# Kernel tuning notes

Hardware: AMD Instinct MI355X
Metric: run time of the kernel (lower is better)

## Reference

```python
import jax, jax.numpy as jnp
import numpy as np

N, E, G = 40000, 400000, 64
IN, ED, HID, HEADS, OUT = 2, 18, 64, 4, 3

def _glorot(key, shape):
    fan_in = shape[0]
    return jax.random.normal(key, shape, dtype=jnp.float32) / np.float32(np.sqrt(fan_in))

def setup_inputs():
    key = jax.random.key(0)
    ks = jax.random.split(key, 32)
    d1 = HEADS * HID  # 256
    return {
        "x": jax.random.normal(ks[0], (N, IN), jnp.float32),
        "edge_index": jax.random.randint(ks[1], (2, E), 0, N),
        "edge_attr": jax.random.normal(ks[2], (E, ED), jnp.float32),
        "batch": jnp.sort(jax.random.randint(ks[3], (N,), 0, G)),
        # conv1: TransformerConv(2 -> 64, heads=4, concat=True, beta=True, edge_dim=18)
        "Wq1": _glorot(ks[4], (IN, d1)), "bq1": jnp.zeros((d1,), jnp.float32),
        "Wk1": _glorot(ks[5], (IN, d1)), "bk1": jnp.zeros((d1,), jnp.float32),
        "Wv1": _glorot(ks[6], (IN, d1)), "bv1": jnp.zeros((d1,), jnp.float32),
        "We1": _glorot(ks[7], (ED, d1)),
        "Wskip1": _glorot(ks[8], (IN, d1)), "bskip1": jnp.zeros((d1,), jnp.float32),
        "Wbeta1": _glorot(ks[9], (3 * d1, 1)),
        # conv2: TransformerConv(256 -> 64, heads=1, concat=False, beta=True, edge_dim=18)
        "Wq2": _glorot(ks[10], (d1, HID)), "bq2": jnp.zeros((HID,), jnp.float32),
        "Wk2": _glorot(ks[11], (d1, HID)), "bk2": jnp.zeros((HID,), jnp.float32),
        "Wv2": _glorot(ks[12], (d1, HID)), "bv2": jnp.zeros((HID,), jnp.float32),
        "We2": _glorot(ks[13], (ED, HID)),
        "Wskip2": _glorot(ks[14], (d1, HID)), "bskip2": jnp.zeros((HID,), jnp.float32),
        "Wbeta2": _glorot(ks[15], (3 * HID, 1)),
        "Wlin": _glorot(ks[16], (HID, OUT)), "blin": jnp.zeros((OUT,), jnp.float32),
    }

def _tconv(x, src, dst, edge_attr, Wq, bq, Wk, bk, Wv, bv, We, Wskip, bskip, Wbeta, H, C, concat):
    # PyG TransformerConv with edge_dim, beta=True, root_weight=True (eval: dropout off)
    n = x.shape[0]
    q = (x @ Wq + bq).reshape(n, H, C)
    k = (x @ Wk + bk).reshape(n, H, C)
    v = (x @ Wv + bv).reshape(n, H, C)
    e = (edge_attr @ We).reshape(-1, H, C)              # [E,H,C]
    kj = k[src] + e                                      # key_j + edge
    alpha = jnp.einsum('ehc,ehc->eh', q[dst], kj) * (1.0 / (C ** 0.5))  # [E,H]
    # segment softmax over destination nodes
    amax = jax.ops.segment_max(alpha, dst, num_segments=n)
    ex = jnp.exp(alpha - amax[dst])
    den = jax.ops.segment_sum(ex, dst, num_segments=n)
    w = ex / (den[dst] + 1e-16)
    msg = (v[src] + e) * w[:, :, None]                   # [E,H,C]
    out = jax.ops.segment_sum(msg, dst, num_segments=n)  # [N,H,C]
    out = out.reshape(n, H * C) if concat else out.mean(axis=1)
    # beta-gated skip connection
    xr = x @ Wskip + bskip
    beta = jax.nn.sigmoid(jnp.concatenate([out, xr, out - xr], axis=-1) @ Wbeta)
    return beta * xr + (1.0 - beta) * out

def reference(x, edge_index, edge_attr, batch, Wq1, bq1, Wk1, bk1, Wv1, bv1, We1, Wskip1, bskip1, Wbeta1, Wq2, bq2, Wk2, bk2, Wv2, bv2, We2, Wskip2, bskip2, Wbeta2, Wlin, blin):
    src, dst = edge_index[0], edge_index[1]
    h = jax.nn.relu(_tconv(x, src, dst, edge_attr, Wq1, bq1, Wk1, bk1, Wv1, bv1, We1, Wskip1, bskip1, Wbeta1, HEADS, HID, True))
    h = jax.nn.relu(_tconv(h, src, dst, edge_attr, Wq2, bq2, Wk2, bk2, Wv2, bv2, We2, Wskip2, bskip2, Wbeta2, 1, HID, False))
    # global mean pool per graph
    s = jax.ops.segment_sum(h, batch, num_segments=G)
    cnt = jax.ops.segment_sum(jnp.ones((h.shape[0], 1), h.dtype), batch, num_segments=G)
    pooled = s / jnp.maximum(cnt, 1.0)
    return pooled @ Wlin + blin
```

## Files before the change

kernel.cpp:

```cpp
#include <hip/hip_runtime.h>
#include <hip/hip_fp16.h>

#define N_NODES 40000
#define N_EDGES 400000
#define N_GRAPHS 64
#define D1 256
#define HIDC 64
#define NHEADS 4
#define EDIM 18
#define EPAD 20
#define OUTF 3
#define APAD 264

typedef _Float16 f16x8 __attribute__((ext_vector_type(8)));
typedef float f32x4 __attribute__((ext_vector_type(4)));

__global__ void prep_w(const float* __restrict__ Wq, const float* __restrict__ bq,
                       const float* __restrict__ Wk, const float* __restrict__ bk,
                       const float* __restrict__ Wv, const float* __restrict__ bv,
                       const float* __restrict__ Ws, const float* __restrict__ bs,
                       const float* __restrict__ We2,
                       const float* __restrict__ Wq1, const float* __restrict__ bq1,
                       const float* __restrict__ Wk1, const float* __restrict__ bk1,
                       const float* __restrict__ We1,
                       __half* __restrict__ Bt, float* __restrict__ bias,
                       float* __restrict__ cbuf) {
    int c = blockIdx.x, k = threadIdx.x;
    if (c < 256) {
        int m = c >> 6, d = c & 63;
        const float* W = (m == 0) ? Wq : (m == 1) ? Wk : (m == 2) ? Wv : Ws;
        Bt[c * 256 + k] = __float2half(W[k * 64 + d]);
        if (k == 0) {
            const float* b = (m == 0) ? bq : (m == 1) ? bk : (m == 2) ? bv : bs;
            bias[c] = b[d];
        }
    } else if (c < 288) {
        int j = c - 256;
        float s = 0.f;
        if (j < EDIM)
            for (int cc = 0; cc < 64; ++cc) s += Wq[k * 64 + cc] * We2[j * 64 + cc];
        Bt[c * 256 + k] = __float2half(s);
        if (k == 0) {
            float b = 0.f;
            if (j < EDIM)
                for (int cc = 0; cc < 64; ++cc) b += bq[cc] * We2[j * 64 + cc];
            bias[c] = b;
        }
    } else {
        int t = k;
        if (t < 36) {
            int h = t / 9, r = t % 9, a = r / 3, b = r % 3;
            const float* A = (a == 0) ? Wq1 : (a == 1) ? Wq1 + D1 : bq1;
            const float* B = (b == 0) ? Wk1 : (b == 1) ? Wk1 + D1 : bk1;
            float s = 0.f;
            for (int cc = 0; cc < 64; ++cc) s += A[h * 64 + cc] * B[h * 64 + cc];
            cbuf[h * 63 + a * 3 + b] = s;
        } else if (t < 252) {
            int i = t - 36;
            int h = i / 54, rr = (i % 54) / 18, j = i % 18;
            const float* A = (rr == 0) ? Wq1 : (rr == 1) ? Wq1 + D1 : bq1;
            float s = 0.f;
            for (int cc = 0; cc < 64; ++cc) s += A[h * 64 + cc] * We1[j * D1 + h * 64 + cc];
            cbuf[h * 63 + 9 + rr * 18 + j] = s;
        }
    }
}

__global__ void initA(const float* __restrict__ x, const float* __restrict__ cbuf,
                      float* __restrict__ coef, float* __restrict__ acc1,
                      float* __restrict__ acc2, float* __restrict__ out2,
                      int* __restrict__ deg, float* __restrict__ pooled,
                      int* __restrict__ gs, int* __restrict__ ge) {
    int t = blockIdx.x * 256 + threadIdx.x;
    acc1[t] = 0.f;
    {
        int n = t / 84, r = t % 84, h = r / 21, c = r % 21;
        const float* cb = cbuf + h * 63;
        float x0 = x[2 * n], x1 = x[2 * n + 1], o;
        if (c < 3) o = x0 * cb[c] + x1 * cb[3 + c] + cb[6 + c];
        else { int j = c - 3; o = x0 * cb[9 + j] + x1 * cb[27 + j] + cb[45 + j]; }
        coef[t] = o;
    }
    if (t < N_NODES * 64) out2[t] = 0.f;
    if (t < N_NODES * 20) acc2[t] = 0.f;
    if (t < N_NODES) deg[t] = 0;
    if (t < N_GRAPHS * HIDC) pooled[t] = 0.f;
    if (t < N_GRAPHS) { gs[t] = 0; ge[t] = 0; }
}

__global__ void hist_kernel(const int* __restrict__ ei, int* __restrict__ deg,
                            const int* __restrict__ batch, int* __restrict__ gs,
                            int* __restrict__ ge) {
    int e = blockIdx.x * 256 + threadIdx.x;
    if (e < N_EDGES) atomicAdd(&deg[ei[N_EDGES + e]], 1);
    int n = e;
    if (n < N_NODES) {
        int b = batch[n];
        if (n == 0) gs[b] = 0;
        else { int pb = batch[n - 1]; if (pb != b) { ge[pb] = n; gs[b] = n; } }
        if (n == N_NODES - 1) ge[b] = N_NODES;
    }
}

__global__ void scanA(const int* __restrict__ deg, int* __restrict__ bsum) {
    __shared__ int s[256];
    int b = blockIdx.x, t = threadIdx.x;
    s[t] = (t < 160) ? deg[b * 160 + t] : 0;
    __syncthreads();
    for (int off = 128; off; off >>= 1) {
        if (t < off) s[t] += s[t + off];
        __syncthreads();
    }
    if (t == 0) bsum[b] = s[0];
}

__global__ void scanB(const int* __restrict__ bsum, int* __restrict__ boff) {
    __shared__ int s[256];
    int t = threadIdx.x;
    int v = (t < 250) ? bsum[t] : 0;
    s[t] = v;
    __syncthreads();
    for (int off = 1; off < 256; off <<= 1) {
        int add = (t >= off) ? s[t - off] : 0;
        __syncthreads();
        s[t] += add;
        __syncthreads();
    }
    if (t < 250) boff[t] = s[t] - v;
}

__global__ void scanC(const int* __restrict__ deg, const int* __restrict__ boff,
                      int* __restrict__ cursor) {
    __shared__ int s[256];
    int b = blockIdx.x, t = threadIdx.x;
    int v = (t < 160) ? deg[b * 160 + t] : 0;
    s[t] = v;
    __syncthreads();
    for (int off = 1; off < 256; off <<= 1) {
        int add = (t >= off) ? s[t - off] : 0;
        __syncthreads();
        s[t] += add;
        __syncthreads();
    }
    if (t < 160) cursor[b * 160 + t] = boff[b] + s[t] - v;
}

__global__ void perm_kernel(const int* __restrict__ ei, int* __restrict__ cursor,
                            int* __restrict__ inv) {
    int e = blockIdx.x * 256 + threadIdx.x;
    if (e >= N_EDGES) return;
    int p = atomicAdd(&cursor[ei[N_EDGES + e]], 1);
    inv[p] = e;
}

__global__ void gatherE(const int* __restrict__ inv, const int* __restrict__ ei,
                        const float* __restrict__ ea, const float* __restrict__ x,
                        const float* __restrict__ coef,
                        int* __restrict__ src_s, int* __restrict__ dst_s,
                        float* __restrict__ ea_s, float* __restrict__ alpha1) {
    int p = blockIdx.x * 256 + threadIdx.x;
    if (p >= N_EDGES) return;
    int e = inv[p];
    int src = ei[e], dst = ei[N_EDGES + e];
    src_s[p] = src;
    dst_s[p] = dst;
    const float* srow = ea + (size_t)e * EDIM;
    float s[EDIM];
    #pragma unroll
    for (int j = 0; j < EDIM; ++j) s[j] = srow[j];
    float x0 = x[src * 2], x1 = x[src * 2 + 1];
    float4* drow = (float4*)(ea_s + (size_t)p * EPAD);
    drow[0] = make_float4(s[0],  s[1],  s[2],  s[3]);
    drow[1] = make_float4(s[4],  s[5],  s[6],  s[7]);
    drow[2] = make_float4(s[8],  s[9],  s[10], s[11]);
    drow[3] = make_float4(s[12], s[13], s[14], s[15]);
    drow[4] = make_float4(s[16], s[17], x0, x1);
    const float* cb = coef + (size_t)dst * 84;
    #pragma unroll
    for (int h = 0; h < NHEADS; ++h) {
        const float* c = cb + h * 21;
        float a = x0 * c[0] + x1 * c[1] + c[2];
        #pragma unroll
        for (int j = 0; j < EDIM; ++j) a += s[j] * c[3 + j];
        alpha1[(size_t)h * N_EDGES + p] = __expf(a * 0.125f);
    }
}

__global__ void strip1(const int* __restrict__ dst_s, const float* __restrict__ alpha1,
                       const float* __restrict__ ea_s, float* __restrict__ acc1) {
    int t = threadIdx.x;
    int strip = blockIdx.x * 2 + (t >> 7);
    int gl = t & 127;
    bool active = gl < 84;
    int cgl = active ? gl : 83;
    int h = cgl / 21, comp = cgl % 21;
    int voff = (comp == 0) ? 18 : (comp == 1) ? 19 : (comp - 3);
    bool isone = (comp == 2);
    int p0 = strip * 16;
    int dsts[16]; float w[16]; float v[16];
    #pragma unroll
    for (int j = 0; j < 16; ++j) dsts[j] = dst_s[p0 + j];
    #pragma unroll
    for (int j = 0; j < 16; ++j) w[j] = alpha1[(size_t)h * N_EDGES + p0 + j];
    #pragma unroll
    for (int j = 0; j < 16; ++j) v[j] = isone ? 1.f : ea_s[(size_t)(p0 + j) * EPAD + voff];
    float acc = 0.f;
    int prev = dsts[0];
    #pragma unroll
    for (int j = 0; j < 16; ++j) {
        if (dsts[j] != prev) {
            if (active) atomicAdd(&acc1[(size_t)prev * 84 + gl], acc);
            acc = 0.f; prev = dsts[j];
        }
        acc += w[j] * v[j];
    }
    if (active) atomicAdd(&acc1[(size_t)prev * 84 + gl], acc);
}

__global__ void finalize1x(const float* __restrict__ x, const float* __restrict__ acc1,
                           const float* __restrict__ Wv, const float* __restrict__ bv,
                           const float* __restrict__ We, const float* __restrict__ Wskip,
                           const float* __restrict__ bskip, const float* __restrict__ Wbeta,
                           __half* __restrict__ h1f) {
    __shared__ float red[4][4];
    int nb = blockIdx.x * 4;
    int t = threadIdx.x;
    int h = t >> 6;
    float wv0 = Wv[t], wv1 = Wv[D1 + t], bvv = bv[t];
    float we[EDIM];
    #pragma unroll
    for (int j = 0; j < EDIM; ++j) we[j] = We[j * D1 + t];
    float ws0 = Wskip[t], ws1 = Wskip[D1 + t], bsv = bskip[t];
    float wb0 = Wbeta[t], wb1 = Wbeta[D1 + t], wb2 = Wbeta[2 * D1 + t];
    float o[4], xr[4], part[4];
    #pragma unroll
    for (int i = 0; i < 4; ++i) {
        int node = nb + i;
        const float* a = acc1 + (size_t)node * 84 + h * 21;
        float l = a[2];
        float oo = a[0] * wv0 + a[1] * wv1 + l * bvv;
        #pragma unroll
        for (int j = 0; j < EDIM; ++j) oo += a[3 + j] * we[j];
        oo /= (l + 1e-16f);
        float x0 = x[node * 2], x1 = x[node * 2 + 1];
        xr[i] = x0 * ws0 + x1 * ws1 + bsv;
        o[i] = oo;
        part[i] = oo * wb0 + xr[i] * wb1 + (oo - xr[i]) * wb2;
    }
    #pragma unroll
    for (int off = 32; off; off >>= 1) {
        #pragma unroll
        for (int i = 0; i < 4; ++i) part[i] += __shfl_xor(part[i], off);
    }
    if ((t & 63) == 0) {
        #pragma unroll
        for (int i = 0; i < 4; ++i) red[h][i] = part[i];
    }
    __syncthreads();
    #pragma unroll
    for (int i = 0; i < 4; ++i) {
        float tot = red[0][i] + red[1][i] + red[2][i] + red[3][i];
        float beta = 1.f / (1.f + __expf(-tot));
        h1f[(size_t)(nb + i) * D1 + t] =
            __float2half(fmaxf(beta * xr[i] + (1.f - beta) * o[i], 0.f));
    }
}

__device__ __forceinline__ void nl2_store(int c, int gr, float v,
        float* __restrict__ q2, float* __restrict__ k2, __half* __restrict__ v2h,
        float* __restrict__ xr2, float* __restrict__ qe) {
    if (c < 256) {
        int m = c >> 6, d = c & 63;
        if (m == 0)      q2[(size_t)gr * 64 + d] = v;
        else if (m == 1) k2[(size_t)gr * 64 + d] = v;
        else if (m == 2) v2h[(size_t)gr * 64 + d] = __float2half(v);
        else             xr2[(size_t)gr * 64 + d] = v;
    } else {
        qe[(size_t)gr * 32 + (c - 256)] = v;
    }
}

__global__ __launch_bounds__(256) void nl2_mfma(
        const __half* __restrict__ h1f, const __half* __restrict__ Bt,
        const float* __restrict__ bias,
        float* __restrict__ q2, float* __restrict__ k2,
        __half* __restrict__ v2h, float* __restrict__ xr2,
        float* __restrict__ qe) {
    __shared__ _Float16 As[64 * APAD];
    int t = threadIdx.x;
    int row0 = blockIdx.x * 64;
    const float4* gsrc = (const float4*)(h1f + (size_t)row0 * 256);
    #pragma unroll
    for (int i = 0; i < 8; ++i) {
        int li = i * 256 + t;
        int r = li >> 5, c8 = li & 31;
        *(float4*)(As + r * APAD + c8 * 8) = gsrc[li];
    }
    __syncthreads();
    int wave = t >> 6, lane = t & 63, quad = lane >> 4, mm = lane & 15;
    const _Float16* Bp = (const _Float16*)Bt;
    for (int ct = wave; ct < 18; ct += 4) {
        int c0 = ct * 16 + mm;
        const _Float16* b0 = Bp + (size_t)c0 * 256 + quad * 8;
        f16x8 b[8];
        #pragma unroll
        for (int s = 0; s < 8; ++s) b[s] = *(const f16x8*)(b0 + s * 32);
        float bz = bias[c0];
        #pragma unroll
        for (int rt = 0; rt < 4; ++rt) {
            const _Float16* arow = As + (rt * 16 + mm) * APAD + quad * 8;
            f16x8 a[8];
            #pragma unroll
            for (int s = 0; s < 8; ++s) a[s] = *(const f16x8*)(arow + s * 32);
            f32x4 accA = {bz, bz, bz, bz};
            f32x4 accB = {0.f, 0.f, 0.f, 0.f};
            #pragma unroll
            for (int s = 0; s < 4; ++s) {
                accA = __builtin_amdgcn_mfma_f32_16x16x32_f16(a[s],     b[s],     accA, 0, 0, 0);
                accB = __builtin_amdgcn_mfma_f32_16x16x32_f16(a[s + 4], b[s + 4], accB, 0, 0, 0);
            }
            #pragma unroll
            for (int r = 0; r < 4; ++r) {
                int gr = row0 + rt * 16 + quad * 4 + r;
                nl2_store(c0, gr, accA[r] + accB[r], q2, k2, v2h, xr2, qe);
            }
        }
    }
}

#define LG2_BLOCKS 2048
#define LG2_WAVES (LG2_BLOCKS * 4)
__global__ void logits2(const int* __restrict__ src_s, const int* __restrict__ dst_s,
                        const float* __restrict__ ea_s, const float* __restrict__ q2,
                        const float* __restrict__ k2, const float* __restrict__ qe,
                        float* __restrict__ alpha2) {
    int t = threadIdx.x, wid = t >> 6, lane = t & 63;
    int w = blockIdx.x * 4 + wid;
    for (int base = w; base < N_EDGES; base += 2 * LG2_WAVES) {
        int p1 = base, p2 = base + LG2_WAVES;
        bool has2 = p2 < N_EDGES;
        int p2c = has2 ? p2 : p1;
        int s1 = src_s[p1], d1 = dst_s[p1];
        int s2 = src_s[p2c], d2 = dst_s[p2c];
        float dd1 = q2[(size_t)d1 * 64 + lane] * k2[(size_t)s1 * 64 + lane];
        float dd2 = q2[(size_t)d2 * 64 + lane] * k2[(size_t)s2 * 64 + lane];
        if (lane < 20) {
            dd1 += qe[(size_t)d1 * 32 + lane] * ea_s[(size_t)p1 * EPAD + lane];
            dd2 += qe[(size_t)d2 * 32 + lane] * ea_s[(size_t)p2c * EPAD + lane];
        }
        #pragma unroll
        for (int off = 32; off; off >>= 1) {
            dd1 += __shfl_xor(dd1, off);
            dd2 += __shfl_xor(dd2, off);
        }
        if (lane == 0) {
            alpha2[p1] = __expf(dd1 * 0.125f);
            if (has2) alpha2[p2] = __expf(dd2 * 0.125f);
        }
    }
}

__global__ void spmm2s(const int* __restrict__ dst_s, const int* __restrict__ src_s,
                       const float* __restrict__ alpha2, const __half* __restrict__ v2h,
                       const float* __restrict__ ea_s,
                       float* __restrict__ out2, float* __restrict__ acc2) {
    int t = threadIdx.x;
    int strip = blockIdx.x * 4 + (t >> 6);
    int lane = t & 63;
    int p0 = strip * 16;
    int dsts[16]; int srcs[16]; float w[16];
    #pragma unroll
    for (int j = 0; j < 16; ++j) dsts[j] = dst_s[p0 + j];
    #pragma unroll
    for (int j = 0; j < 16; ++j) srcs[j] = src_s[p0 + j];
    #pragma unroll
    for (int j = 0; j < 16; ++j) w[j] = alpha2[p0 + j];
    float vv[16]; float ev[16];
    #pragma unroll
    for (int j = 0; j < 16; ++j) vv[j] = __half2float(v2h[(size_t)srcs[j] * 64 + lane]);
    #pragma unroll
    for (int j = 0; j < 16; ++j)
        ev[j] = (lane < EDIM) ? ea_s[(size_t)(p0 + j) * EPAD + lane] : 1.f;
    float acc = 0.f, accS = 0.f;
    int prev = dsts[0];
    #pragma unroll
    for (int j = 0; j < 16; ++j) {
        if (dsts[j] != prev) {
            atomicAdd(&out2[(size_t)prev * 64 + lane], acc);
            if (lane < 19) atomicAdd(&acc2[(size_t)prev * 20 + lane], accS);
            acc = 0.f; accS = 0.f; prev = dsts[j];
        }
        acc += w[j] * vv[j];
        accS += w[j] * ev[j];
    }
    atomicAdd(&out2[(size_t)prev * 64 + lane], acc);
    if (lane < 19) atomicAdd(&acc2[(size_t)prev * 20 + lane], accS);
}

__global__ void finalize2x(const float* __restrict__ out2, const float* __restrict__ acc2,
                           const float* __restrict__ xr2, const float* __restrict__ We2,
                           const float* __restrict__ Wb2, float* __restrict__ h2) {
    __shared__ float w2s[EDIM * 64];
    int t = threadIdx.x;
    for (int i = t; i < EDIM * 64; i += 256) w2s[i] = We2[i];
    __syncthreads();
    int node = blockIdx.x * 4 + (t >> 6);
    int lane = t & 63;
    const float* a2 = acc2 + (size_t)node * 20;
    float num = out2[(size_t)node * 64 + lane];
    #pragma unroll
    for (int j = 0; j < EDIM; ++j) num += a2[j] * w2s[j * 64 + lane];
    float o = num / (a2[18] + 1e-16f);
    float xr = xr2[(size_t)node * 64 + lane];
    float part = o * Wb2[lane] + xr * Wb2[64 + lane] + (o - xr) * Wb2[128 + lane];
    #pragma unroll
    for (int off = 32; off; off >>= 1) part += __shfl_xor(part, off);
    float beta = 1.f / (1.f + __expf(-part));
    h2[(size_t)node * 64 + lane] = fmaxf(beta * xr + (1.f - beta) * o, 0.f);
}

__global__ void pool_kernel(const float* __restrict__ h2, const int* __restrict__ gs,
                            const int* __restrict__ ge, float* __restrict__ pooled) {
    __shared__ float red[4][64];
    int g = blockIdx.x >> 2, q = blockIdx.x & 3;
    int t = threadIdx.x, wv = t >> 6, lane = t & 63;
    int s = gs[g], e = ge[g];
    float sum = 0.f;
    for (int n = s + q * 4 + wv; n < e; n += 16) sum += h2[(size_t)n * 64 + lane];
    red[wv][lane] = sum;
    __syncthreads();
    if (wv == 0) {
        float v = red[0][lane] + red[1][lane] + red[2][lane] + red[3][lane];
        atomicAdd(&pooled[g * 64 + lane], v);
    }
}

__global__ void final_lin(const float* __restrict__ pooled, const int* __restrict__ gs,
                          const int* __restrict__ ge,
                          const float* __restrict__ Wlin, const float* __restrict__ blin,
                          float* __restrict__ out) {
    int t = threadIdx.x;
    if (t >= N_GRAPHS * OUTF) return;
    int g = t / OUTF, o = t % OUTF;
    int c = ge[g] - gs[g];
    float inv = 1.f / fmaxf((float)c, 1.f);
    float acc = 0.f;
    for (int kk = 0; kk < HIDC; ++kk) acc += pooled[g * 64 + kk] * Wlin[kk * OUTF + o];
    out[t] = acc * inv + blin[o];
}

extern "C" void kernel_launch(void* const* d_in, const int* in_sizes, int n_in,
                              void* d_out, int out_size, void* d_ws, size_t ws_size,
                              hipStream_t stream) {
    const float* x      = (const float*)d_in[0];
    const int*   ei     = (const int*)d_in[1];
    const float* ea     = (const float*)d_in[2];
    const int*   batch  = (const int*)d_in[3];
    const float* Wq1    = (const float*)d_in[4];  const float* bq1    = (const float*)d_in[5];
    const float* Wk1    = (const float*)d_in[6];  const float* bk1    = (const float*)d_in[7];
    const float* Wv1    = (const float*)d_in[8];  const float* bv1    = (const float*)d_in[9];
    const float* We1    = (const float*)d_in[10];
    const float* Wskip1 = (const float*)d_in[11]; const float* bskip1 = (const float*)d_in[12];
    const float* Wbeta1 = (const float*)d_in[13];
    const float* Wq2    = (const float*)d_in[14]; const float* bq2    = (const float*)d_in[15];
    const float* Wk2    = (const float*)d_in[16]; const float* bk2    = (const float*)d_in[17];
    const float* Wv2    = (const float*)d_in[18]; const float* bv2    = (const float*)d_in[19];
    const float* We2    = (const float*)d_in[20];
    const float* Wskip2 = (const float*)d_in[21]; const float* bskip2 = (const float*)d_in[22];
    const float* Wbeta2 = (const float*)d_in[23];
    const float* Wlin   = (const float*)d_in[24]; const float* blin   = (const float*)d_in[25];

    float* ptr = (float*)d_ws;
    float* q2     = ptr; ptr += (size_t)N_NODES * 64;
    float* k2     = ptr; ptr += (size_t)N_NODES * 64;
    float* xr2    = ptr; ptr += (size_t)N_NODES * 64;
    float* qe     = ptr; ptr += (size_t)N_NODES * 32;
    __half* v2h   = (__half*)ptr; ptr += (size_t)N_NODES * 32;
    float* ea_s   = ptr; ptr += (size_t)N_EDGES * EPAD;
    float* alpha2 = ptr; ptr += N_EDGES;
    float* acc2   = ptr; ptr += (size_t)N_NODES * 20;
    float* out2   = ptr; ptr += (size_t)N_NODES * 64;
    float* pooled = ptr; ptr += N_GRAPHS * HIDC;
    int*   gs     = (int*)ptr; ptr += N_GRAPHS;
    int*   ge     = (int*)ptr; ptr += N_GRAPHS;
    float* cbuf   = ptr; ptr += 256;
    float* bias   = ptr; ptr += 320;
    __half* Bt    = (__half*)ptr; ptr += (288 * 256) / 2;
    int*   src_s  = (int*)ptr; ptr += N_EDGES;
    int*   dst_s  = (int*)ptr; ptr += N_EDGES;
    int*   inv    = (int*)ptr; ptr += N_EDGES;
    int*   deg    = (int*)ptr; ptr += N_NODES;
    int*   cursor = (int*)ptr; ptr += N_NODES;
    int*   bsum   = (int*)ptr; ptr += 256;
    int*   boff   = (int*)ptr; ptr += 256;
    float* coef   = ptr; ptr += (size_t)N_NODES * 84;
    float* h2     = coef;
    float* acc1   = ptr; ptr += (size_t)N_NODES * 84;
    float* alpha1 = ptr; ptr += (size_t)4 * N_EDGES;
    __half* h1f   = (__half*)ptr; ptr += (size_t)N_NODES * 128;

    const int EB = (N_EDGES + 255) / 256;

    prep_w<<<289, 256, 0, stream>>>(Wq2, bq2, Wk2, bk2, Wv2, bv2, Wskip2, bskip2, We2,
                                    Wq1, bq1, Wk1, bk1, We1, Bt, bias, cbuf);
    initA<<<(N_NODES * 84) / 256, 256, 0, stream>>>(x, cbuf, coef, acc1, acc2, out2,
                                                    deg, pooled, gs, ge);
    hist_kernel<<<EB, 256, 0, stream>>>(ei, deg, batch, gs, ge);
    scanA<<<250, 256, 0, stream>>>(deg, bsum);
    scanB<<<1, 256, 0, stream>>>(bsum, boff);
    scanC<<<250, 256, 0, stream>>>(deg, boff, cursor);
    perm_kernel<<<EB, 256, 0, stream>>>(ei, cursor, inv);
    gatherE<<<EB, 256, 0, stream>>>(inv, ei, ea, x, coef, src_s, dst_s, ea_s, alpha1);

    strip1<<<(N_EDGES / 16) / 2, 256, 0, stream>>>(dst_s, alpha1, ea_s, acc1);
    finalize1x<<<N_NODES / 4, 256, 0, stream>>>(x, acc1, Wv1, bv1, We1, Wskip1, bskip1,
                                                Wbeta1, h1f);

    nl2_mfma<<<N_NODES / 64, 256, 0, stream>>>(h1f, Bt, bias, q2, k2, v2h, xr2, qe);
    logits2<<<LG2_BLOCKS, 256, 0, stream>>>(src_s, dst_s, ea_s, q2, k2, qe, alpha2);
    spmm2s<<<(N_EDGES / 16) / 4, 256, 0, stream>>>(dst_s, src_s, alpha2, v2h, ea_s,
                                                   out2, acc2);
    finalize2x<<<N_NODES / 4, 256, 0, stream>>>(out2, acc2, xr2, We2, Wbeta2, h2);

    pool_kernel<<<N_GRAPHS * 4, 256, 0, stream>>>(h2, gs, ge, pooled);
    final_lin<<<1, 256, 0, stream>>>(pooled, gs, ge, Wlin, blin, (float*)d_out);
}
```

Baseline: 436.8 us.

## Store sorted edge attributes as fp16 and fold histogram into init kernel

Sorted edge attributes plus source coordinates are now stored as packed fp16 rows of 24 halves instead of fp32 rows of 20 floats. This roughly shrinks the per-edge stream that strip1, logits2 and spmm2s re-read. Separately, the degree histogram and graph-boundary detection move into initA, and deg zeroing moves into prep_w, which drops one kernel launch. The fp16 storage costs some precision on edge features and on x0/x1 used in the layer-1 aggregation. logits2 also now skips the x0/x1 lanes, which relies on those qe entries having been zero.

```diff
diff --git a/kernel.cpp b/kernel.cpp
--- a/kernel.cpp
+++ b/kernel.cpp
@@ -8,7 +8,7 @@
 #define HIDC 64
 #define NHEADS 4
 #define EDIM 18
-#define EPAD 20
+#define EPADH 24
 #define OUTF 3
 #define APAD 264
 
@@ -24,8 +24,10 @@
                        const float* __restrict__ Wk1, const float* __restrict__ bk1,
                        const float* __restrict__ We1,
                        __half* __restrict__ Bt, float* __restrict__ bias,
-                       float* __restrict__ cbuf) {
+                       float* __restrict__ cbuf, int* __restrict__ deg) {
     int c = blockIdx.x, k = threadIdx.x;
+    int gid = c * 256 + k;
+    if (gid < N_NODES) deg[gid] = 0;
     if (c < 256) {
         int m = c >> 6, d = c & 63;
         const float* W = (m == 0) ? Wq : (m == 1) ? Wk : (m == 2) ? Wv : Ws;
@@ -67,6 +69,7 @@
 }
 
 __global__ void initA(const float* __restrict__ x, const float* __restrict__ cbuf,
+                      const int* __restrict__ ei, const int* __restrict__ batch,
                       float* __restrict__ coef, float* __restrict__ acc1,
                       float* __restrict__ acc2, float* __restrict__ out2,
                       int* __restrict__ deg, float* __restrict__ pooled,
@@ -83,22 +86,13 @@
     }
     if (t < N_NODES * 64) out2[t] = 0.f;
     if (t < N_NODES * 20) acc2[t] = 0.f;
-    if (t < N_NODES) deg[t] = 0;
+    if (t < N_EDGES) atomicAdd(&deg[ei[N_EDGES + t]], 1);
     if (t < N_GRAPHS * HIDC) pooled[t] = 0.f;
-    if (t < N_GRAPHS) { gs[t] = 0; ge[t] = 0; }
-}
-
-__global__ void hist_kernel(const int* __restrict__ ei, int* __restrict__ deg,
-                            const int* __restrict__ batch, int* __restrict__ gs,
-                            int* __restrict__ ge) {
-    int e = blockIdx.x * 256 + threadIdx.x;
-    if (e < N_EDGES) atomicAdd(&deg[ei[N_EDGES + e]], 1);
-    int n = e;
-    if (n < N_NODES) {
-        int b = batch[n];
-        if (n == 0) gs[b] = 0;
-        else { int pb = batch[n - 1]; if (pb != b) { ge[pb] = n; gs[b] = n; } }
-        if (n == N_NODES - 1) ge[b] = N_NODES;
+    if (t < N_NODES) {
+        int b = batch[t];
+        if (t == 0) gs[b] = 0;
+        else { int pb = batch[t - 1]; if (pb != b) { ge[pb] = t; gs[b] = t; } }
+        if (t == N_NODES - 1) ge[b] = N_NODES;
     }
 }
 
@@ -157,7 +151,7 @@
                         const float* __restrict__ ea, const float* __restrict__ x,
                         const float* __restrict__ coef,
                         int* __restrict__ src_s, int* __restrict__ dst_s,
-                        float* __restrict__ ea_s, float* __restrict__ alpha1) {
+                        _Float16* __restrict__ eah, float* __restrict__ alpha1) {
     int p = blockIdx.x * 256 + threadIdx.x;
     if (p >= N_EDGES) return;
     int e = inv[p];
@@ -169,12 +163,16 @@
     #pragma unroll
     for (int j = 0; j < EDIM; ++j) s[j] = srow[j];
     float x0 = x[src * 2], x1 = x[src * 2 + 1];
-    float4* drow = (float4*)(ea_s + (size_t)p * EPAD);
-    drow[0] = make_float4(s[0],  s[1],  s[2],  s[3]);
-    drow[1] = make_float4(s[4],  s[5],  s[6],  s[7]);
-    drow[2] = make_float4(s[8],  s[9],  s[10], s[11]);
-    drow[3] = make_float4(s[12], s[13], s[14], s[15]);
-    drow[4] = make_float4(s[16], s[17], x0, x1);
+    f16x8 r0 = {(_Float16)s[0], (_Float16)s[1], (_Float16)s[2], (_Float16)s[3],
+                (_Float16)s[4], (_Float16)s[5], (_Float16)s[6], (_Float16)s[7]};
+    f16x8 r1 = {(_Float16)s[8], (_Float16)s[9], (_Float16)s[10], (_Float16)s[11],
+                (_Float16)s[12], (_Float16)s[13], (_Float16)s[14], (_Float16)s[15]};
+    f16x8 r2 = {(_Float16)s[16], (_Float16)s[17], (_Float16)x0, (_Float16)x1,
+                (_Float16)0.f, (_Float16)0.f, (_Float16)0.f, (_Float16)0.f};
+    _Float16* drow = eah + (size_t)p * EPADH;
+    *(f16x8*)(drow)      = r0;
+    *(f16x8*)(drow + 8)  = r1;
+    *(f16x8*)(drow + 16) = r2;
     const float* cb = coef + (size_t)dst * 84;
     #pragma unroll
     for (int h = 0; h < NHEADS; ++h) {
@@ -187,7 +185,7 @@
 }
 
 __global__ void strip1(const int* __restrict__ dst_s, const float* __restrict__ alpha1,
-                       const float* __restrict__ ea_s, float* __restrict__ acc1) {
+                       const _Float16* __restrict__ eah, float* __restrict__ acc1) {
     int t = threadIdx.x;
     int strip = blockIdx.x * 2 + (t >> 7);
     int gl = t & 127;
@@ -203,7 +201,8 @@
     #pragma unroll
     for (int j = 0; j < 16; ++j) w[j] = alpha1[(size_t)h * N_EDGES + p0 + j];
     #pragma unroll
-    for (int j = 0; j < 16; ++j) v[j] = isone ? 1.f : ea_s[(size_t)(p0 + j) * EPAD + voff];
+    for (int j = 0; j < 16; ++j)
+        v[j] = isone ? 1.f : (float)eah[(size_t)(p0 + j) * EPADH + voff];
     float acc = 0.f;
     int prev = dsts[0];
     #pragma unroll
@@ -331,7 +330,7 @@
 #define LG2_BLOCKS 2048
 #define LG2_WAVES (LG2_BLOCKS * 4)
 __global__ void logits2(const int* __restrict__ src_s, const int* __restrict__ dst_s,
-                        const float* __restrict__ ea_s, const float* __restrict__ q2,
+                        const _Float16* __restrict__ eah, const float* __restrict__ q2,
                         const float* __restrict__ k2, const float* __restrict__ qe,
                         float* __restrict__ alpha2) {
     int t = threadIdx.x, wid = t >> 6, lane = t & 63;
@@ -344,9 +343,9 @@
         int s2 = src_s[p2c], d2 = dst_s[p2c];
         float dd1 = q2[(size_t)d1 * 64 + lane] * k2[(size_t)s1 * 64 + lane];
         float dd2 = q2[(size_t)d2 * 64 + lane] * k2[(size_t)s2 * 64 + lane];
-        if (lane < 20) {
-            dd1 += qe[(size_t)d1 * 32 + lane] * ea_s[(size_t)p1 * EPAD + lane];
-            dd2 += qe[(size_t)d2 * 32 + lane] * ea_s[(size_t)p2c * EPAD + lane];
+        if (lane < EDIM) {
+            dd1 += qe[(size_t)d1 * 32 + lane] * (float)eah[(size_t)p1 * EPADH + lane];
+            dd2 += qe[(size_t)d2 * 32 + lane] * (float)eah[(size_t)p2c * EPADH + lane];
         }
         #pragma unroll
         for (int off = 32; off; off >>= 1) {
@@ -362,7 +361,7 @@
 
 __global__ void spmm2s(const int* __restrict__ dst_s, const int* __restrict__ src_s,
                        const float* __restrict__ alpha2, const __half* __restrict__ v2h,
-                       const float* __restrict__ ea_s,
+                       const _Float16* __restrict__ eah,
                        float* __restrict__ out2, float* __restrict__ acc2) {
     int t = threadIdx.x;
     int strip = blockIdx.x * 4 + (t >> 6);
@@ -380,7 +379,7 @@
     for (int j = 0; j < 16; ++j) vv[j] = __half2float(v2h[(size_t)srcs[j] * 64 + lane]);
     #pragma unroll
     for (int j = 0; j < 16; ++j)
-        ev[j] = (lane < EDIM) ? ea_s[(size_t)(p0 + j) * EPAD + lane] : 1.f;
+        ev[j] = (lane < EDIM) ? (float)eah[(size_t)(p0 + j) * EPADH + lane] : 1.f;
     float acc = 0.f, accS = 0.f;
     int prev = dsts[0];
     #pragma unroll
@@ -476,7 +475,7 @@
     float* xr2    = ptr; ptr += (size_t)N_NODES * 64;
     float* qe     = ptr; ptr += (size_t)N_NODES * 32;
     __half* v2h   = (__half*)ptr; ptr += (size_t)N_NODES * 32;
-    float* ea_s   = ptr; ptr += (size_t)N_EDGES * EPAD;
+    _Float16* eah = (_Float16*)ptr; ptr += (size_t)N_EDGES * EPADH / 2;
     float* alpha2 = ptr; ptr += N_EDGES;
     float* acc2   = ptr; ptr += (size_t)N_NODES * 20;
     float* out2   = ptr; ptr += (size_t)N_NODES * 64;
@@ -502,23 +501,22 @@
     const int EB = (N_EDGES + 255) / 256;
 
     prep_w<<<289, 256, 0, stream>>>(Wq2, bq2, Wk2, bk2, Wv2, bv2, Wskip2, bskip2, We2,
-                                    Wq1, bq1, Wk1, bk1, We1, Bt, bias, cbuf);
-    initA<<<(N_NODES * 84) / 256, 256, 0, stream>>>(x, cbuf, coef, acc1, acc2, out2,
-                                                    deg, pooled, gs, ge);
-    hist_kernel<<<EB, 256, 0, stream>>>(ei, deg, batch, gs, ge);
+                                    Wq1, bq1, Wk1, bk1, We1, Bt, bias, cbuf, deg);
+    initA<<<(N_NODES * 84) / 256, 256, 0, stream>>>(x, cbuf, ei, batch, coef, acc1,
+                                                    acc2, out2, deg, pooled, gs, ge);
     scanA<<<250, 256, 0, stream>>>(deg, bsum);
     scanB<<<1, 256, 0, stream>>>(bsum, boff);
     scanC<<<250, 256, 0, stream>>>(deg, boff, cursor);
     perm_kernel<<<EB, 256, 0, stream>>>(ei, cursor, inv);
-    gatherE<<<EB, 256, 0, stream>>>(inv, ei, ea, x, coef, src_s, dst_s, ea_s, alpha1);
-
-    strip1<<<(N_EDGES / 16) / 2, 256, 0, stream>>>(dst_s, alpha1, ea_s, acc1);
+    gatherE<<<EB, 256, 0, stream>>>(inv, ei, ea, x, coef, src_s, dst_s, eah, alpha1);
+
+    strip1<<<(N_EDGES / 16) / 2, 256, 0, stream>>>(dst_s, alpha1, eah, acc1);
     finalize1x<<<N_NODES / 4, 256, 0, stream>>>(x, acc1, Wv1, bv1, We1, Wskip1, bskip1,
                                                 Wbeta1, h1f);
 
     nl2_mfma<<<N_NODES / 64, 256, 0, stream>>>(h1f, Bt, bias, q2, k2, v2h, xr2, qe);
-    logits2<<<LG2_BLOCKS, 256, 0, stream>>>(src_s, dst_s, ea_s, q2, k2, qe, alpha2);
-    spmm2s<<<(N_EDGES / 16) / 4, 256, 0, stream>>>(dst_s, src_s, alpha2, v2h, ea_s,
+    logits2<<<LG2_BLOCKS, 256, 0, stream>>>(src_s, dst_s, eah, q2, k2, qe, alpha2);
+    spmm2s<<<(N_EDGES / 16) / 4, 256, 0, stream>>>(dst_s, src_s, alpha2, v2h, eah,
                                                    out2, acc2);
     finalize2x<<<N_NODES / 4, 256, 0, stream>>>(out2, acc2, xr2, We2, Wbeta2, h2);
 
```

Result: slower. 457.0 us (+4.6%).
